# Performance work log

Measured on AMD Instinct MI355X. Metric: run time of the kernel, lower is better.

## Reference

```python
import jax, jax.numpy as jnp
import numpy as np

E = 1_000_000      # number of edges
T = 2_000_000      # number of angle triplets
EDGE_DIM = 64
HIDDEN = 128
LN_EPS = 1e-5


def _layer_norm(x, gamma, beta):
    mu = jnp.mean(x, axis=-1, keepdims=True)
    var = jnp.mean(jnp.square(x - mu), axis=-1, keepdims=True)
    return (x - mu) * jax.lax.rsqrt(var + LN_EPS) * gamma + beta


def setup_inputs() -> dict:
    key = jax.random.key(0)
    ks = jax.random.split(key, 8)
    in_dim = 2 * EDGE_DIM + 4  # 132

    def lin(k, fan_in, fan_out):
        bound = 1.0 / np.sqrt(fan_in)
        kw, kb = jax.random.split(k)
        W = jax.random.uniform(kw, (fan_in, fan_out), jnp.float32, -bound, bound)
        b = jax.random.uniform(kb, (fan_out,), jnp.float32, -bound, bound)
        return W, b

    W1, b1 = lin(ks[0], in_dim, HIDDEN)
    W2, b2 = lin(ks[1], HIDDEN, HIDDEN)
    W3, b3 = lin(ks[2], HIDDEN, EDGE_DIM)

    return {
        "edge_feat": jax.random.normal(ks[3], (E, EDGE_DIM), jnp.float32),
        "triplet_idx": jax.random.randint(ks[4], (T, 2), 0, E, jnp.int64) if jax.config.jax_enable_x64 else jax.random.randint(ks[4], (T, 2), 0, E, jnp.int32),
        "triplet_geo": jax.random.uniform(ks[5], (T, 4), jnp.float32),
        "W1": W1, "b1": b1,
        "g1": jnp.ones((HIDDEN,), jnp.float32), "be1": jnp.zeros((HIDDEN,), jnp.float32),
        "W2": W2, "b2": b2,
        "g2": jnp.ones((HIDDEN,), jnp.float32), "be2": jnp.zeros((HIDDEN,), jnp.float32),
        "W3": W3, "b3": b3,
        "gn": jnp.ones((EDGE_DIM,), jnp.float32), "bn": jnp.zeros((EDGE_DIM,), jnp.float32),
    }


def reference(edge_feat, triplet_idx, triplet_geo,
              W1, b1, g1, be1, W2, b2, g2, be2, W3, b3, gn, bn):
    num_edges = edge_feat.shape[0]
    e_ij = triplet_idx[:, 0]
    e_kj = triplet_idx[:, 1]

    f_ij = edge_feat[e_ij]                      # [T, edge_dim] gather
    f_kj = edge_feat[e_kj]                      # [T, edge_dim] gather
    x = jnp.concatenate([f_ij, f_kj, triplet_geo], axis=1)  # [T, 2*edge_dim+4]

    # mlp_phi: Linear -> SiLU -> LayerNorm -> Linear -> SiLU -> LayerNorm
    h = _layer_norm(jax.nn.silu(x @ W1 + b1), g1, be1)
    m = _layer_norm(jax.nn.silu(h @ W2 + b2), g2, be2)  # [T, hidden]

    # scatter-mean over e_ij with dim_size = num_edges
    sums = jax.ops.segment_sum(m, e_ij, num_segments=num_edges)
    cnts = jax.ops.segment_sum(jnp.ones((m.shape[0],), m.dtype), e_ij, num_segments=num_edges)
    agg = sums / jnp.maximum(cnts, 1.0)[:, None]         # [E, hidden]

    out = edge_feat + (agg @ W3 + b3)
    return _layer_norm(out, gn, bn)
```

## Files before the change

### kernel.cpp

```cpp
#include <hip/hip_runtime.h>
#include <hip/hip_bf16.h>
#include <stdint.h>

typedef __attribute__((ext_vector_type(8))) short short8;
typedef __attribute__((ext_vector_type(4))) float f32x4;
typedef unsigned short u16;

#define OFF_PSUM 0ULL
#define OFF_CNT  256000000ULL
#define OFF_EBF  260000000ULL
#define OFF_WP1  388000000ULL
#define OFF_WP2  (OFF_WP1 + 40960ULL)
#define OFF_WP3  (OFF_WP2 + 32768ULL)
#define OFF_S2   (OFF_WP3 + 16384ULL)
#define OFF_C2   (OFF_S2 + 512ULL)
#define OFF_S3   (OFF_C2 + 512ULL)
#define OFF_T3   (OFF_S3 + 256ULL)

#define LDS_P1S 40960
#define LDS_P1Q 43008
#define LDS_P2S 45056
#define LDS_P2Q 47104
#define LDS_EIJ 49152
#define LDS_EKJ 49664
#define LDS_TOTAL 50176

__device__ __forceinline__ u16 f2bf(float f) {
  union { float f; uint32_t u; } c; c.f = f;
  uint32_t u = c.u;
  return (u16)((u + 0x7FFFu + ((u >> 16) & 1u)) >> 16);
}
__device__ __forceinline__ float silu(float y) {
  return y / (1.0f + __expf(-y));
}

#define MFMA16(a, b, c) __builtin_amdgcn_mfma_f32_16x16x32_bf16((a), (b), (c), 0, 0, 0)


__global__ __launch_bounds__(256) void k_conv_edge(const float* __restrict__ ef,
                                                   u16* __restrict__ ebf) {
  int i = blockIdx.x * 256 + threadIdx.x;
  float4 v = ((const float4*)ef)[i];
  ushort4 o;
  o.x = f2bf(v.x); o.y = f2bf(v.y); o.z = f2bf(v.z); o.w = f2bf(v.w);
  ((ushort4*)ebf)[i] = o;
}

__global__ __launch_bounds__(256) void k_pack_w(const float* __restrict__ W1,
                                                const float* __restrict__ W2,
                                                const float* __restrict__ W3,
                                                const float* __restrict__ g1,
                                                const float* __restrict__ g2,
                                                u16* __restrict__ wp1,
                                                u16* __restrict__ wp2,
                                                u16* __restrict__ wp3) {
  int i = blockIdx.x * 256 + threadIdx.x;
  if (i < 20480) {
    int j = i & 7, n = (i >> 3) & 127, kb = i >> 10;
    int k = kb * 8 + j;
    wp1[i] = (k < 132) ? f2bf(W1[k * 128 + n]) : (u16)0;
  } else if (i < 36864) {
    int i2 = i - 20480;
    int j = i2 & 7, n = (i2 >> 3) & 127, kb = i2 >> 10;
    int k = kb * 8 + j;
    wp2[i2] = f2bf(g1[k] * W2[k * 128 + n]);
  } else if (i < 45056) {
    int i3 = i - 36864;
    int j = i3 & 7, n = (i3 >> 3) & 63, kb = i3 >> 9;
    int k = kb * 8 + j;
    wp3[i3] = f2bf(g2[k] * W3[k * 64 + n]);
  }
}

__global__ __launch_bounds__(256) void k_pack_vec(
    const float* __restrict__ W2, const float* __restrict__ W3,
    const float* __restrict__ g1, const float* __restrict__ be1, const float* __restrict__ b2,
    const float* __restrict__ g2, const float* __restrict__ be2,
    float* __restrict__ s2, float* __restrict__ c2,
    float* __restrict__ s3, float* __restrict__ t3) {
  int t = threadIdx.x;
  if (t < 128) {
    float a = 0.f, b = 0.f;
    for (int k = 0; k < 128; ++k) {
      float w = W2[k * 128 + t];
      a += g1[k] * w; b += be1[k] * w;
    }
    s2[t] = a; c2[t] = b + b2[t];
  } else if (t < 192) {
    int n = t - 128;
    float a = 0.f, b = 0.f;
    for (int k = 0; k < 128; ++k) {
      float w = W3[k * 64 + n];
      a += g2[k] * w; b += be2[k] * w;
    }
    s3[n] = a; t3[n] = b;
  }
}


__global__ __launch_bounds__(512, 4) void k_triplet(
    const u16* __restrict__ ebf, const int* __restrict__ tidx,
    const float* __restrict__ geo,
    const u16* __restrict__ wp1, const u16* __restrict__ wp2, const u16* __restrict__ wp3,
    const float* __restrict__ b1,
    const float* __restrict__ s2v, const float* __restrict__ c2v,
    const float* __restrict__ s3v,
    float* __restrict__ psum, float* __restrict__ cnt) {
  extern __shared__ char smem[];
  float* P1S = (float*)(smem + LDS_P1S);
  float* P1Q = (float*)(smem + LDS_P1Q);
  float* P2S = (float*)(smem + LDS_P2S);
  float* P2Q = (float*)(smem + LDS_P2Q);
  int* EIJ = (int*)(smem + LDS_EIJ);
  int* EKJ = (int*)(smem + LDS_EKJ);

  const int tid = threadIdx.x;
  const int wave = tid >> 6, lane = tid & 63;
  const int wm = wave >> 2, wn = wave & 3;
  const int l15 = lane & 15, lg = lane >> 4;
  const int t0 = blockIdx.x * 128;
  const int n0 = wn * 32 + l15;
  const int n3 = wn * 16 + l15;
  const int rowA = wm * 64 + l15;

  const short8* wb1 = (const short8*)wp1;
  short8 w1f[10];
#pragma unroll
  for (int s5 = 0; s5 < 5; ++s5) {
    int kb = s5 * 4 + lg;
    w1f[2 * s5] = wb1[kb * 128 + n0];
    w1f[2 * s5 + 1] = wb1[kb * 128 + n0 + 16];
  }
  float b1c0 = b1[n0], b1c1 = b1[n0 + 16];

  if (tid < 128) {
    int2 p = ((const int2*)tidx)[t0 + tid];
    EIJ[tid] = p.x; EKJ[tid] = p.y;
    atomicAdd(&cnt[p.x], 1.0f);
  }
  __syncthreads();

  {
    const int r = tid >> 2, s = tid & 3;
    const int e = (s < 2) ? EIJ[r] : EKJ[r];
    const uint4* src = (const uint4*)(ebf + (size_t)e * 64) + (s & 1) * 4;
    uint4 v0 = src[0], v1 = src[1], v2 = src[2], v3 = src[3];
    const int swz = (r & 7) << 4;
    char* rowp = smem + r * 320;
    *(uint4*)(rowp + ((s * 64 + 0) ^ swz)) = v0;
    *(uint4*)(rowp + ((s * 64 + 16) ^ swz)) = v1;
    *(uint4*)(rowp + ((s * 64 + 32) ^ swz)) = v2;
    *(uint4*)(rowp + ((s * 64 + 48) ^ swz)) = v3;
    if (s == 0) {
      float4 gq = ((const float4*)geo)[t0 + r];
      ushort4 gb;
      gb.x = f2bf(gq.x); gb.y = f2bf(gq.y); gb.z = f2bf(gq.z); gb.w = f2bf(gq.w);
      *(ushort4*)(rowp + 256) = gb;
      *(uint2*)(rowp + 264) = (uint2){0, 0};
    } else {
      *(uint4*)(rowp + 256 + s * 16) = (uint4){0, 0, 0, 0};
    }
  }
  __syncthreads();

  f32x4 acc[4][2];
#pragma unroll
  for (int mf = 0; mf < 4; ++mf) { acc[mf][0] = (f32x4)0.f; acc[mf][1] = (f32x4)0.f; }
#pragma unroll
  for (int s5 = 0; s5 < 5; ++s5) {
    short8 a[4];
#pragma unroll
    for (int mf = 0; mf < 4; ++mf) {
      int row = rowA + mf * 16;
      int off = s5 * 64 + lg * 16;
      if (s5 < 4) off ^= (row & 7) << 4;
      a[mf] = *(const short8*)(smem + row * 320 + off);
    }
#pragma unroll
    for (int mf = 0; mf < 4; ++mf) {
      acc[mf][0] = MFMA16(a[mf], w1f[2 * s5], acc[mf][0]);
      acc[mf][1] = MFMA16(a[mf], w1f[2 * s5 + 1], acc[mf][1]);
    }
  }

#pragma unroll
  for (int mf = 0; mf < 4; ++mf)
#pragma unroll
    for (int q = 0; q < 4; ++q) {
      float v0 = silu(acc[mf][0][q] + b1c0);
      float v1 = silu(acc[mf][1][q] + b1c1);
      acc[mf][0][q] = v0; acc[mf][1][q] = v1;
      float ps = v0 + v1, pq = v0 * v0 + v1 * v1;
      ps += __shfl_xor(ps, 1); pq += __shfl_xor(pq, 1);
      ps += __shfl_xor(ps, 2); pq += __shfl_xor(pq, 2);
      ps += __shfl_xor(ps, 4); pq += __shfl_xor(pq, 4);
      ps += __shfl_xor(ps, 8); pq += __shfl_xor(pq, 8);
      if (l15 == 0) {
        int row = wm * 64 + mf * 16 + lg * 4 + q;
        P1S[row * 4 + wn] = ps; P1Q[row * 4 + wn] = pq;
      }
    }
  __syncthreads();

  const short8* wb2 = (const short8*)wp2;
  short8 w2f[8];
#pragma unroll
  for (int s4 = 0; s4 < 4; ++s4) {
    int kb = s4 * 4 + lg;
    w2f[2 * s4] = wb2[kb * 128 + n0];
    w2f[2 * s4 + 1] = wb2[kb * 128 + n0 + 16];
  }
  float s2c0 = s2v[n0], s2c1 = s2v[n0 + 16];
  float c2c0 = c2v[n0], c2c1 = c2v[n0 + 16];

#pragma unroll
  for (int mf = 0; mf < 4; ++mf)
#pragma unroll
    for (int f = 0; f < 2; ++f)
#pragma unroll
      for (int q = 0; q < 4; ++q) {
        int row = wm * 64 + mf * 16 + lg * 4 + q;
        int cb = (wn * 32 + f * 16 + l15) << 1;
        *(u16*)(smem + row * 256 + (cb ^ ((row & 7) << 4))) = f2bf(acc[mf][f][q]);
      }
  __syncthreads();

#pragma unroll
  for (int mf = 0; mf < 4; ++mf) { acc[mf][0] = (f32x4)0.f; acc[mf][1] = (f32x4)0.f; }
#pragma unroll
  for (int s4 = 0; s4 < 4; ++s4) {
    short8 a[4];
#pragma unroll
    for (int mf = 0; mf < 4; ++mf) {
      int row = rowA + mf * 16;
      a[mf] = *(const short8*)(smem + row * 256 + ((s4 * 64 + lg * 16) ^ ((row & 7) << 4)));
    }
#pragma unroll
    for (int mf = 0; mf < 4; ++mf) {
      acc[mf][0] = MFMA16(a[mf], w2f[2 * s4], acc[mf][0]);
      acc[mf][1] = MFMA16(a[mf], w2f[2 * s4 + 1], acc[mf][1]);
    }
  }

#pragma unroll
  for (int mf = 0; mf < 4; ++mf)
#pragma unroll
    for (int q = 0; q < 4; ++q) {
      int row = wm * 64 + mf * 16 + lg * 4 + q;
      float4 sv = *(const float4*)&P1S[row * 4];
      float4 qv = *(const float4*)&P1Q[row * 4];
      float sum = sv.x + sv.y + sv.z + sv.w;
      float sq = qv.x + qv.y + qv.z + qv.w;
      float mu = sum * 0.0078125f;
      float inv = rsqrtf(fmaxf(sq * 0.0078125f - mu * mu, 0.f) + 1e-5f);
      float f0 = inv * (acc[mf][0][q] - mu * s2c0) + c2c0;
      float f1 = inv * (acc[mf][1][q] - mu * s2c1) + c2c1;
      float v0 = silu(f0), v1 = silu(f1);
      acc[mf][0][q] = v0; acc[mf][1][q] = v1;
      float ps = v0 + v1, pq = v0 * v0 + v1 * v1;
      ps += __shfl_xor(ps, 1); pq += __shfl_xor(pq, 1);
      ps += __shfl_xor(ps, 2); pq += __shfl_xor(pq, 2);
      ps += __shfl_xor(ps, 4); pq += __shfl_xor(pq, 4);
      ps += __shfl_xor(ps, 8); pq += __shfl_xor(pq, 8);
      if (l15 == 0) { P2S[row * 4 + wn] = ps; P2Q[row * 4 + wn] = pq; }
    }

  const short8* wb3 = (const short8*)wp3;
  short8 w3f[4];
#pragma unroll
  for (int s4 = 0; s4 < 4; ++s4) w3f[s4] = wb3[(s4 * 4 + lg) * 64 + n3];
  float s3c = s3v[n3];

  __syncthreads();

#pragma unroll
  for (int mf = 0; mf < 4; ++mf)
#pragma unroll
    for (int f = 0; f < 2; ++f)
#pragma unroll
      for (int q = 0; q < 4; ++q) {
        int row = wm * 64 + mf * 16 + lg * 4 + q;
        int cb = (wn * 32 + f * 16 + l15) << 1;
        *(u16*)(smem + row * 256 + (cb ^ ((row & 7) << 4))) = f2bf(acc[mf][f][q]);
      }
  __syncthreads();

  f32x4 acc3[4];
#pragma unroll
  for (int mf = 0; mf < 4; ++mf) acc3[mf] = (f32x4)0.f;
#pragma unroll
  for (int s4 = 0; s4 < 4; ++s4) {
    short8 a[4];
#pragma unroll
    for (int mf = 0; mf < 4; ++mf) {
      int row = rowA + mf * 16;
      a[mf] = *(const short8*)(smem + row * 256 + ((s4 * 64 + lg * 16) ^ ((row & 7) << 4)));
    }
#pragma unroll
    for (int mf = 0; mf < 4; ++mf) acc3[mf] = MFMA16(a[mf], w3f[s4], acc3[mf]);
  }
#pragma unroll
  for (int mf = 0; mf < 4; ++mf)
#pragma unroll
    for (int q = 0; q < 4; ++q) {
      int row = wm * 64 + mf * 16 + lg * 4 + q;
      float4 sv = *(const float4*)&P2S[row * 4];
      float4 qv = *(const float4*)&P2Q[row * 4];
      float sum = sv.x + sv.y + sv.z + sv.w;
      float sq = qv.x + qv.y + qv.z + qv.w;
      float mu = sum * 0.0078125f;
      float inv = rsqrtf(fmaxf(sq * 0.0078125f - mu * mu, 0.f) + 1e-5f);
      float y = inv * (acc3[mf][q] - mu * s3c);
      int e = EIJ[row];
      atomicAdd(psum + (size_t)e * 64 + n3, y);
    }
}


__global__ __launch_bounds__(256) void k_final(
    const float* __restrict__ psum, const float* __restrict__ cnt,
    const float* __restrict__ ef, const float* __restrict__ b3,
    const float* __restrict__ t3, const float* __restrict__ gn,
    const float* __restrict__ bn, float* __restrict__ out) {
  int g = blockIdx.x * 256 + threadIdx.x;
  int e = g >> 2, s = g & 3;
  float cv = cnt[e];
  float ic = 1.0f / fmaxf(cv, 1.0f);
  float tw = (cv > 0.f) ? 1.0f : 0.0f;
  float x[16];
  const float4* ps = (const float4*)(psum + (size_t)e * 64 + s * 16);
  const float4* fe = (const float4*)(ef + (size_t)e * 64 + s * 16);
  const float4* p3 = (const float4*)(b3 + s * 16);
  const float4* pt = (const float4*)(t3 + s * 16);
#pragma unroll
  for (int i = 0; i < 4; ++i) {
    float4 a = ps[i], b = fe[i], c = p3[i], d = pt[i];
    x[4 * i + 0] = b.x + a.x * ic + c.x + tw * d.x;
    x[4 * i + 1] = b.y + a.y * ic + c.y + tw * d.y;
    x[4 * i + 2] = b.z + a.z * ic + c.z + tw * d.z;
    x[4 * i + 3] = b.w + a.w * ic + c.w + tw * d.w;
  }
  float sum = 0.f, ss = 0.f;
#pragma unroll
  for (int i = 0; i < 16; ++i) { sum += x[i]; ss += x[i] * x[i]; }
  sum += __shfl_xor(sum, 1); ss += __shfl_xor(ss, 1);
  sum += __shfl_xor(sum, 2); ss += __shfl_xor(ss, 2);
  float mu = sum * (1.0f / 64.0f);
  float inv = rsqrtf(ss * (1.0f / 64.0f) - mu * mu + 1e-5f);
  float4* po = (float4*)(out + (size_t)e * 64 + s * 16);
#pragma unroll
  for (int i = 0; i < 4; ++i) {
    float4 gv = ((const float4*)(gn + s * 16))[i];
    float4 bv = ((const float4*)(bn + s * 16))[i];
    float4 o;
    o.x = (x[4 * i + 0] - mu) * inv * gv.x + bv.x;
    o.y = (x[4 * i + 1] - mu) * inv * gv.y + bv.y;
    o.z = (x[4 * i + 2] - mu) * inv * gv.z + bv.z;
    o.w = (x[4 * i + 3] - mu) * inv * gv.w + bv.w;
    po[i] = o;
  }
}

extern "C" void kernel_launch(void* const* d_in, const int* in_sizes, int n_in,
                              void* d_out, int out_size, void* d_ws, size_t ws_size,
                              hipStream_t stream) {
  const float* edge_feat = (const float*)d_in[0];
  const int* tidx = (const int*)d_in[1];
  const float* geo = (const float*)d_in[2];
  const float* W1 = (const float*)d_in[3];
  const float* b1 = (const float*)d_in[4];
  const float* g1 = (const float*)d_in[5];
  const float* be1 = (const float*)d_in[6];
  const float* W2 = (const float*)d_in[7];
  const float* b2 = (const float*)d_in[8];
  const float* g2 = (const float*)d_in[9];
  const float* be2 = (const float*)d_in[10];
  const float* W3 = (const float*)d_in[11];
  const float* b3 = (const float*)d_in[12];
  const float* gn = (const float*)d_in[13];
  const float* bn = (const float*)d_in[14];

  char* ws = (char*)d_ws;
  float* psum = (float*)(ws + OFF_PSUM);
  float* cnt = (float*)(ws + OFF_CNT);
  u16* ebf = (u16*)(ws + OFF_EBF);
  u16* wp1 = (u16*)(ws + OFF_WP1);
  u16* wp2 = (u16*)(ws + OFF_WP2);
  u16* wp3 = (u16*)(ws + OFF_WP3);
  float* s2 = (float*)(ws + OFF_S2);
  float* c2 = (float*)(ws + OFF_C2);
  float* s3 = (float*)(ws + OFF_S3);
  float* t3 = (float*)(ws + OFF_T3);
  float* out = (float*)d_out;

  hipMemsetAsync(ws, 0, 260000000ULL, stream);
  k_conv_edge<<<62500, 256, 0, stream>>>(edge_feat, ebf);
  k_pack_w<<<176, 256, 0, stream>>>(W1, W2, W3, g1, g2, wp1, wp2, wp3);
  k_pack_vec<<<1, 256, 0, stream>>>(W2, W3, g1, be1, b2, g2, be2, s2, c2, s3, t3);

  k_triplet<<<15625, 512, LDS_TOTAL, stream>>>(ebf, tidx, geo, wp1, wp2, wp3,
                                               b1, s2, c2, s3, psum, cnt);
  k_final<<<15625, 256, 0, stream>>>(psum, cnt, edge_feat, b3, t3, gn, bn, out);
}
```

Before: 1.077 ms.

## Transpose triplet MLP GEMMs so weights are the A operand and triplets are columns

Restructures the fused triplet MLP so each MFMA treats the weight matrix as the A operand and the triplets as the N dimension. Hidden activations are written to LDS as packed bf16 pairs, and the intermediate layer gets its own buffer, which removes one barrier. LayerNorm statistics now reduce with two cross-lane shuffles instead of four per row. Weights are loaded from global memory inside each k-step instead of being held in registers, and LDS use grows from about 50KB to about 79KB per block, which may lower occupancy. It also switches SiLU to a reciprocal approximation and uses packed bf16 conversion.

```diff
diff --git a/kernel.cpp b/kernel.cpp
--- a/kernel.cpp
+++ b/kernel.cpp
@@ -9,29 +9,37 @@
 #define OFF_PSUM 0ULL
 #define OFF_CNT  256000000ULL
 #define OFF_EBF  260000000ULL
-#define OFF_WP1  388000000ULL
-#define OFF_WP2  (OFF_WP1 + 40960ULL)
-#define OFF_WP3  (OFF_WP2 + 32768ULL)
-#define OFF_S2   (OFF_WP3 + 16384ULL)
+#define OFF_WT1  388000000ULL
+#define OFF_WT2  (OFF_WT1 + 40960ULL)
+#define OFF_WT3  (OFF_WT2 + 32768ULL)
+#define OFF_S2   (OFF_WT3 + 16384ULL)
 #define OFF_C2   (OFF_S2 + 512ULL)
 #define OFF_S3   (OFF_C2 + 512ULL)
 #define OFF_T3   (OFF_S3 + 256ULL)
 
-#define LDS_P1S 40960
-#define LDS_P1Q 43008
-#define LDS_P2S 45056
-#define LDS_P2Q 47104
-#define LDS_EIJ 49152
-#define LDS_EKJ 49664
-#define LDS_TOTAL 50176
+#define LDS_X   0
+#define LDS_H   40960
+#define LDS_P1S 73728
+#define LDS_P1Q 74752
+#define LDS_P2S 75776
+#define LDS_P2Q 76800
+#define LDS_EIJ 77824
+#define LDS_EKJ 78336
+#define LDS_TOTAL 78848
 
 __device__ __forceinline__ u16 f2bf(float f) {
   union { float f; uint32_t u; } c; c.f = f;
   uint32_t u = c.u;
   return (u16)((u + 0x7FFFu + ((u >> 16) & 1u)) >> 16);
 }
+__device__ __forceinline__ uint32_t pkbf(float lo, float hi) {
+  float2 t; t.x = lo; t.y = hi;
+  __hip_bfloat162 h = __float22bfloat162_rn(t);
+  uint32_t u; __builtin_memcpy(&u, &h, 4);
+  return u;
+}
 __device__ __forceinline__ float silu(float y) {
-  return y / (1.0f + __expf(-y));
+  return y * __builtin_amdgcn_rcpf(1.0f + __expf(-y));
 }
 
 #define MFMA16(a, b, c) __builtin_amdgcn_mfma_f32_16x16x32_bf16((a), (b), (c), 0, 0, 0)
@@ -51,24 +59,21 @@
                                                 const float* __restrict__ W3,
                                                 const float* __restrict__ g1,
                                                 const float* __restrict__ g2,
-                                                u16* __restrict__ wp1,
-                                                u16* __restrict__ wp2,
-                                                u16* __restrict__ wp3) {
+                                                u16* __restrict__ wt1,
+                                                u16* __restrict__ wt2,
+                                                u16* __restrict__ wt3) {
   int i = blockIdx.x * 256 + threadIdx.x;
   if (i < 20480) {
-    int j = i & 7, n = (i >> 3) & 127, kb = i >> 10;
-    int k = kb * 8 + j;
-    wp1[i] = (k < 132) ? f2bf(W1[k * 128 + n]) : (u16)0;
+    int n = i / 160, k = i - n * 160;
+    wt1[i] = (k < 132) ? f2bf(W1[k * 128 + n]) : (u16)0;
   } else if (i < 36864) {
     int i2 = i - 20480;
-    int j = i2 & 7, n = (i2 >> 3) & 127, kb = i2 >> 10;
-    int k = kb * 8 + j;
-    wp2[i2] = f2bf(g1[k] * W2[k * 128 + n]);
+    int n = i2 >> 7, k = i2 & 127;
+    wt2[i2] = f2bf(g1[k] * W2[k * 128 + n]);
   } else if (i < 45056) {
     int i3 = i - 36864;
-    int j = i3 & 7, n = (i3 >> 3) & 63, kb = i3 >> 9;
-    int k = kb * 8 + j;
-    wp3[i3] = f2bf(g2[k] * W3[k * 64 + n]);
+    int n = i3 >> 7, k = i3 & 127;
+    wt3[i3] = f2bf(g2[k] * W3[k * 64 + n]);
   }
 }
 
@@ -101,7 +106,7 @@
 __global__ __launch_bounds__(512, 4) void k_triplet(
     const u16* __restrict__ ebf, const int* __restrict__ tidx,
     const float* __restrict__ geo,
-    const u16* __restrict__ wp1, const u16* __restrict__ wp2, const u16* __restrict__ wp3,
+    const u16* __restrict__ wt1, const u16* __restrict__ wt2, const u16* __restrict__ wt3,
     const float* __restrict__ b1,
     const float* __restrict__ s2v, const float* __restrict__ c2v,
     const float* __restrict__ s3v,
@@ -119,19 +124,6 @@
   const int wm = wave >> 2, wn = wave & 3;
   const int l15 = lane & 15, lg = lane >> 4;
   const int t0 = blockIdx.x * 128;
-  const int n0 = wn * 32 + l15;
-  const int n3 = wn * 16 + l15;
-  const int rowA = wm * 64 + l15;
-
-  const short8* wb1 = (const short8*)wp1;
-  short8 w1f[10];
-#pragma unroll
-  for (int s5 = 0; s5 < 5; ++s5) {
-    int kb = s5 * 4 + lg;
-    w1f[2 * s5] = wb1[kb * 128 + n0];
-    w1f[2 * s5 + 1] = wb1[kb * 128 + n0 + 16];
-  }
-  float b1c0 = b1[n0], b1c1 = b1[n0 + 16];
 
   if (tid < 128) {
     int2 p = ((const int2*)tidx)[t0 + tid];
@@ -151,14 +143,16 @@
     *(uint4*)(rowp + ((s * 64 + 16) ^ swz)) = v1;
     *(uint4*)(rowp + ((s * 64 + 32) ^ swz)) = v2;
     *(uint4*)(rowp + ((s * 64 + 48) ^ swz)) = v3;
+    const int tswz = (r & 3) << 4;
     if (s == 0) {
       float4 gq = ((const float4*)geo)[t0 + r];
-      ushort4 gb;
-      gb.x = f2bf(gq.x); gb.y = f2bf(gq.y); gb.z = f2bf(gq.z); gb.w = f2bf(gq.w);
-      *(ushort4*)(rowp + 256) = gb;
-      *(uint2*)(rowp + 264) = (uint2){0, 0};
+      uint2 gw;
+      gw.x = pkbf(gq.x, gq.y); gw.y = pkbf(gq.z, gq.w);
+      char* tp = rowp + 256 + (0 ^ tswz);
+      *(uint2*)tp = gw;
+      *(uint2*)(tp + 8) = (uint2){0, 0};
     } else {
-      *(uint4*)(rowp + 256 + s * 16) = (uint4){0, 0, 0, 0};
+      *(uint4*)(rowp + 256 + ((s * 16) ^ tswz)) = (uint4){0, 0, 0, 0};
     }
   }
   __syncthreads();
@@ -166,154 +160,197 @@
   f32x4 acc[4][2];
 #pragma unroll
   for (int mf = 0; mf < 4; ++mf) { acc[mf][0] = (f32x4)0.f; acc[mf][1] = (f32x4)0.f; }
+  const short8* w1p = (const short8*)wt1;
 #pragma unroll
   for (int s5 = 0; s5 < 5; ++s5) {
-    short8 a[4];
+    short8 aw[4], bx[2];
+#pragma unroll
+    for (int mf = 0; mf < 4; ++mf)
+      aw[mf] = w1p[(wm * 64 + mf * 16 + l15) * 20 + s5 * 4 + lg];
+#pragma unroll
+    for (int f = 0; f < 2; ++f) {
+      int trip = wn * 32 + f * 16 + l15;
+      int off;
+      if (s5 < 4) off = (s5 * 64 + lg * 16) ^ ((trip & 7) << 4);
+      else off = 256 + ((lg * 16) ^ ((trip & 3) << 4));
+      bx[f] = *(const short8*)(smem + trip * 320 + off);
+    }
 #pragma unroll
     for (int mf = 0; mf < 4; ++mf) {
-      int row = rowA + mf * 16;
-      int off = s5 * 64 + lg * 16;
-      if (s5 < 4) off ^= (row & 7) << 4;
-      a[mf] = *(const short8*)(smem + row * 320 + off);
+      acc[mf][0] = MFMA16(aw[mf], bx[0], acc[mf][0]);
+      acc[mf][1] = MFMA16(aw[mf], bx[1], acc[mf][1]);
+    }
+  }
+
+  {
+    float4 b1f[4];
+#pragma unroll
+    for (int mf = 0; mf < 4; ++mf)
+      b1f[mf] = *(const float4*)(b1 + wm * 64 + mf * 16 + lg * 4);
+    float st[2] = {0.f, 0.f}, sq[2] = {0.f, 0.f};
+#pragma unroll
+    for (int mf = 0; mf < 4; ++mf)
+#pragma unroll
+      for (int f = 0; f < 2; ++f)
+#pragma unroll
+        for (int q = 0; q < 4; ++q) {
+          float v = silu(acc[mf][f][q] + b1f[mf][q]);
+          acc[mf][f][q] = v;
+          st[f] += v; sq[f] += v * v;
+        }
+#pragma unroll
+    for (int f = 0; f < 2; ++f) {
+      st[f] += __shfl_xor(st[f], 16); sq[f] += __shfl_xor(sq[f], 16);
+      st[f] += __shfl_xor(st[f], 32); sq[f] += __shfl_xor(sq[f], 32);
+    }
+    if (lg == 0) {
+#pragma unroll
+      for (int f = 0; f < 2; ++f) {
+        int trip = wn * 32 + f * 16 + l15;
+        P1S[trip * 2 + wm] = st[f];
+        P1Q[trip * 2 + wm] = sq[f];
+      }
+    }
+#pragma unroll
+    for (int mf = 0; mf < 4; ++mf)
+#pragma unroll
+      for (int f = 0; f < 2; ++f) {
+        int trip = wn * 32 + f * 16 + l15;
+        uint2 w;
+        w.x = pkbf(acc[mf][f][0], acc[mf][f][1]);
+        w.y = pkbf(acc[mf][f][2], acc[mf][f][3]);
+        *(uint2*)(smem + LDS_H + trip * 256 +
+                  ((wm * 128 + mf * 32 + lg * 8) ^ ((trip & 7) << 4))) = w;
+      }
+  }
+  __syncthreads();
+
+#pragma unroll
+  for (int mf = 0; mf < 4; ++mf) { acc[mf][0] = (f32x4)0.f; acc[mf][1] = (f32x4)0.f; }
+  const short8* w2p = (const short8*)wt2;
+#pragma unroll
+  for (int s4 = 0; s4 < 4; ++s4) {
+    short8 aw[4], bx[2];
+#pragma unroll
+    for (int mf = 0; mf < 4; ++mf)
+      aw[mf] = w2p[(wm * 64 + mf * 16 + l15) * 16 + s4 * 4 + lg];
+#pragma unroll
+    for (int f = 0; f < 2; ++f) {
+      int trip = wn * 32 + f * 16 + l15;
+      bx[f] = *(const short8*)(smem + LDS_H + trip * 256 +
+                               ((s4 * 64 + lg * 16) ^ ((trip & 7) << 4)));
     }
 #pragma unroll
     for (int mf = 0; mf < 4; ++mf) {
-      acc[mf][0] = MFMA16(a[mf], w1f[2 * s5], acc[mf][0]);
-      acc[mf][1] = MFMA16(a[mf], w1f[2 * s5 + 1], acc[mf][1]);
-    }
-  }
-
-#pragma unroll
-  for (int mf = 0; mf < 4; ++mf)
-#pragma unroll
-    for (int q = 0; q < 4; ++q) {
-      float v0 = silu(acc[mf][0][q] + b1c0);
-      float v1 = silu(acc[mf][1][q] + b1c1);
-      acc[mf][0][q] = v0; acc[mf][1][q] = v1;
-      float ps = v0 + v1, pq = v0 * v0 + v1 * v1;
-      ps += __shfl_xor(ps, 1); pq += __shfl_xor(pq, 1);
-      ps += __shfl_xor(ps, 2); pq += __shfl_xor(pq, 2);
-      ps += __shfl_xor(ps, 4); pq += __shfl_xor(pq, 4);
-      ps += __shfl_xor(ps, 8); pq += __shfl_xor(pq, 8);
-      if (l15 == 0) {
-        int row = wm * 64 + mf * 16 + lg * 4 + q;
-        P1S[row * 4 + wn] = ps; P1Q[row * 4 + wn] = pq;
+      acc[mf][0] = MFMA16(aw[mf], bx[0], acc[mf][0]);
+      acc[mf][1] = MFMA16(aw[mf], bx[1], acc[mf][1]);
+    }
+  }
+
+  {
+    float4 s2f[4], c2f[4];
+#pragma unroll
+    for (int mf = 0; mf < 4; ++mf) {
+      s2f[mf] = *(const float4*)(s2v + wm * 64 + mf * 16 + lg * 4);
+      c2f[mf] = *(const float4*)(c2v + wm * 64 + mf * 16 + lg * 4);
+    }
+    float mu[2], inv[2];
+#pragma unroll
+    for (int f = 0; f < 2; ++f) {
+      int trip = wn * 32 + f * 16 + l15;
+      float sm = P1S[trip * 2] + P1S[trip * 2 + 1];
+      float qq = P1Q[trip * 2] + P1Q[trip * 2 + 1];
+      mu[f] = sm * 0.0078125f;
+      inv[f] = rsqrtf(fmaxf(qq * 0.0078125f - mu[f] * mu[f], 0.f) + 1e-5f);
+    }
+    float st[2] = {0.f, 0.f}, sq[2] = {0.f, 0.f};
+#pragma unroll
+    for (int mf = 0; mf < 4; ++mf)
+#pragma unroll
+      for (int f = 0; f < 2; ++f)
+#pragma unroll
+        for (int q = 0; q < 4; ++q) {
+          float y = inv[f] * (acc[mf][f][q] - mu[f] * s2f[mf][q]) + c2f[mf][q];
+          float v = silu(y);
+          acc[mf][f][q] = v;
+          st[f] += v; sq[f] += v * v;
+        }
+#pragma unroll
+    for (int f = 0; f < 2; ++f) {
+      st[f] += __shfl_xor(st[f], 16); sq[f] += __shfl_xor(sq[f], 16);
+      st[f] += __shfl_xor(st[f], 32); sq[f] += __shfl_xor(sq[f], 32);
+    }
+    if (lg == 0) {
+#pragma unroll
+      for (int f = 0; f < 2; ++f) {
+        int trip = wn * 32 + f * 16 + l15;
+        P2S[trip * 2 + wm] = st[f];
+        P2Q[trip * 2 + wm] = sq[f];
       }
     }
+#pragma unroll
+    for (int mf = 0; mf < 4; ++mf)
+#pragma unroll
+      for (int f = 0; f < 2; ++f) {
+        int trip = wn * 32 + f * 16 + l15;
+        uint2 w;
+        w.x = pkbf(acc[mf][f][0], acc[mf][f][1]);
+        w.y = pkbf(acc[mf][f][2], acc[mf][f][3]);
+        *(uint2*)(smem + trip * 256 +
+                  ((wm * 128 + mf * 32 + lg * 8) ^ ((trip & 7) << 4))) = w;
+      }
+  }
   __syncthreads();
 
-  const short8* wb2 = (const short8*)wp2;
-  short8 w2f[8];
+  f32x4 acc3[2][2];
+#pragma unroll
+  for (int mf = 0; mf < 2; ++mf) { acc3[mf][0] = (f32x4)0.f; acc3[mf][1] = (f32x4)0.f; }
+  const short8* w3p = (const short8*)wt3;
 #pragma unroll
   for (int s4 = 0; s4 < 4; ++s4) {
-    int kb = s4 * 4 + lg;
-    w2f[2 * s4] = wb2[kb * 128 + n0];
-    w2f[2 * s4 + 1] = wb2[kb * 128 + n0 + 16];
-  }
-  float s2c0 = s2v[n0], s2c1 = s2v[n0 + 16];
-  float c2c0 = c2v[n0], c2c1 = c2v[n0 + 16];
-
-#pragma unroll
-  for (int mf = 0; mf < 4; ++mf)
-#pragma unroll
-    for (int f = 0; f < 2; ++f)
-#pragma unroll
-      for (int q = 0; q < 4; ++q) {
-        int row = wm * 64 + mf * 16 + lg * 4 + q;
-        int cb = (wn * 32 + f * 16 + l15) << 1;
-        *(u16*)(smem + row * 256 + (cb ^ ((row & 7) << 4))) = f2bf(acc[mf][f][q]);
-      }
-  __syncthreads();
-
-#pragma unroll
-  for (int mf = 0; mf < 4; ++mf) { acc[mf][0] = (f32x4)0.f; acc[mf][1] = (f32x4)0.f; }
-#pragma unroll
-  for (int s4 = 0; s4 < 4; ++s4) {
-    short8 a[4];
-#pragma unroll
-    for (int mf = 0; mf < 4; ++mf) {
-      int row = rowA + mf * 16;
-      a[mf] = *(const short8*)(smem + row * 256 + ((s4 * 64 + lg * 16) ^ ((row & 7) << 4)));
-    }
-#pragma unroll
-    for (int mf = 0; mf < 4; ++mf) {
-      acc[mf][0] = MFMA16(a[mf], w2f[2 * s4], acc[mf][0]);
-      acc[mf][1] = MFMA16(a[mf], w2f[2 * s4 + 1], acc[mf][1]);
-    }
-  }
-
-#pragma unroll
-  for (int mf = 0; mf < 4; ++mf)
-#pragma unroll
-    for (int q = 0; q < 4; ++q) {
-      int row = wm * 64 + mf * 16 + lg * 4 + q;
-      float4 sv = *(const float4*)&P1S[row * 4];
-      float4 qv = *(const float4*)&P1Q[row * 4];
-      float sum = sv.x + sv.y + sv.z + sv.w;
-      float sq = qv.x + qv.y + qv.z + qv.w;
-      float mu = sum * 0.0078125f;
-      float inv = rsqrtf(fmaxf(sq * 0.0078125f - mu * mu, 0.f) + 1e-5f);
-      float f0 = inv * (acc[mf][0][q] - mu * s2c0) + c2c0;
-      float f1 = inv * (acc[mf][1][q] - mu * s2c1) + c2c1;
-      float v0 = silu(f0), v1 = silu(f1);
-      acc[mf][0][q] = v0; acc[mf][1][q] = v1;
-      float ps = v0 + v1, pq = v0 * v0 + v1 * v1;
-      ps += __shfl_xor(ps, 1); pq += __shfl_xor(pq, 1);
-      ps += __shfl_xor(ps, 2); pq += __shfl_xor(pq, 2);
-      ps += __shfl_xor(ps, 4); pq += __shfl_xor(pq, 4);
-      ps += __shfl_xor(ps, 8); pq += __shfl_xor(pq, 8);
-      if (l15 == 0) { P2S[row * 4 + wn] = ps; P2Q[row * 4 + wn] = pq; }
-    }
-
-  const short8* wb3 = (const short8*)wp3;
-  short8 w3f[4];
-#pragma unroll
-  for (int s4 = 0; s4 < 4; ++s4) w3f[s4] = wb3[(s4 * 4 + lg) * 64 + n3];
-  float s3c = s3v[n3];
-
-  __syncthreads();
-
-#pragma unroll
-  for (int mf = 0; mf < 4; ++mf)
-#pragma unroll
-    for (int f = 0; f < 2; ++f)
-#pragma unroll
-      for (int q = 0; q < 4; ++q) {
-        int row = wm * 64 + mf * 16 + lg * 4 + q;
-        int cb = (wn * 32 + f * 16 + l15) << 1;
-        *(u16*)(smem + row * 256 + (cb ^ ((row & 7) << 4))) = f2bf(acc[mf][f][q]);
-      }
-  __syncthreads();
-
-  f32x4 acc3[4];
-#pragma unroll
-  for (int mf = 0; mf < 4; ++mf) acc3[mf] = (f32x4)0.f;
-#pragma unroll
-  for (int s4 = 0; s4 < 4; ++s4) {
-    short8 a[4];
-#pragma unroll
-    for (int mf = 0; mf < 4; ++mf) {
-      int row = rowA + mf * 16;
-      a[mf] = *(const short8*)(smem + row * 256 + ((s4 * 64 + lg * 16) ^ ((row & 7) << 4)));
-    }
-#pragma unroll
-    for (int mf = 0; mf < 4; ++mf) acc3[mf] = MFMA16(a[mf], w3f[s4], acc3[mf]);
-  }
-#pragma unroll
-  for (int mf = 0; mf < 4; ++mf)
-#pragma unroll
-    for (int q = 0; q < 4; ++q) {
-      int row = wm * 64 + mf * 16 + lg * 4 + q;
-      float4 sv = *(const float4*)&P2S[row * 4];
-      float4 qv = *(const float4*)&P2Q[row * 4];
-      float sum = sv.x + sv.y + sv.z + sv.w;
-      float sq = qv.x + qv.y + qv.z + qv.w;
-      float mu = sum * 0.0078125f;
-      float inv = rsqrtf(fmaxf(sq * 0.0078125f - mu * mu, 0.f) + 1e-5f);
-      float y = inv * (acc3[mf][q] - mu * s3c);
-      int e = EIJ[row];
-      atomicAdd(psum + (size_t)e * 64 + n3, y);
-    }
+    short8 aw[2], bx[2];
+#pragma unroll
+    for (int mf = 0; mf < 2; ++mf)
+      aw[mf] = w3p[(wm * 32 + mf * 16 + l15) * 16 + s4 * 4 + lg];
+#pragma unroll
+    for (int f = 0; f < 2; ++f) {
+      int trip = wn * 32 + f * 16 + l15;
+      bx[f] = *(const short8*)(smem + trip * 256 +
+                               ((s4 * 64 + lg * 16) ^ ((trip & 7) << 4)));
+    }
+#pragma unroll
+    for (int mf = 0; mf < 2; ++mf) {
+      acc3[mf][0] = MFMA16(aw[mf], bx[0], acc3[mf][0]);
+      acc3[mf][1] = MFMA16(aw[mf], bx[1], acc3[mf][1]);
+    }
+  }
+  {
+    float4 s3f[2];
+#pragma unroll
+    for (int mf = 0; mf < 2; ++mf)
+      s3f[mf] = *(const float4*)(s3v + wm * 32 + mf * 16 + lg * 4);
+    float mu3[2], inv3[2];
+    int ei[2];
+#pragma unroll
+    for (int f = 0; f < 2; ++f) {
+      int trip = wn * 32 + f * 16 + l15;
+      float sm = P2S[trip * 2] + P2S[trip * 2 + 1];
+      float qq = P2Q[trip * 2] + P2Q[trip * 2 + 1];
+      mu3[f] = sm * 0.0078125f;
+      inv3[f] = rsqrtf(fmaxf(qq * 0.0078125f - mu3[f] * mu3[f], 0.f) + 1e-5f);
+      ei[f] = EIJ[trip];
+    }
+#pragma unroll
+    for (int mf = 0; mf < 2; ++mf)
+#pragma unroll
+      for (int f = 0; f < 2; ++f)
+#pragma unroll
+        for (int q = 0; q < 4; ++q) {
+          float y = inv3[f] * (acc3[mf][f][q] - mu3[f] * s3f[mf][q]);
+          int n3 = wm * 32 + mf * 16 + lg * 4 + q;
+          atomicAdd(psum + (size_t)ei[f] * 64 + n3, y);
+        }
+  }
 }
 
 
@@ -384,9 +421,9 @@
   float* psum = (float*)(ws + OFF_PSUM);
   float* cnt = (float*)(ws + OFF_CNT);
   u16* ebf = (u16*)(ws + OFF_EBF);
-  u16* wp1 = (u16*)(ws + OFF_WP1);
-  u16* wp2 = (u16*)(ws + OFF_WP2);
-  u16* wp3 = (u16*)(ws + OFF_WP3);
+  u16* wt1 = (u16*)(ws + OFF_WT1);
+  u16* wt2 = (u16*)(ws + OFF_WT2);
+  u16* wt3 = (u16*)(ws + OFF_WT3);
   float* s2 = (float*)(ws + OFF_S2);
   float* c2 = (float*)(ws + OFF_C2);
   float* s3 = (float*)(ws + OFF_S3);
@@ -395,10 +432,12 @@
 
   hipMemsetAsync(ws, 0, 260000000ULL, stream);
   k_conv_edge<<<62500, 256, 0, stream>>>(edge_feat, ebf);
-  k_pack_w<<<176, 256, 0, stream>>>(W1, W2, W3, g1, g2, wp1, wp2, wp3);
+  k_pack_w<<<176, 256, 0, stream>>>(W1, W2, W3, g1, g2, wt1, wt2, wt3);
   k_pack_vec<<<1, 256, 0, stream>>>(W2, W3, g1, be1, b2, g2, be2, s2, c2, s3, t3);
 
-  k_triplet<<<15625, 512, LDS_TOTAL, stream>>>(ebf, tidx, geo, wp1, wp2, wp3,
+  hipFuncSetAttribute((const void*)k_triplet,
+                      hipFuncAttributeMaxDynamicSharedMemorySize, LDS_TOTAL);
+  k_triplet<<<15625, 512, LDS_TOTAL, stream>>>(ebf, tidx, geo, wt1, wt2, wt3,
                                                b1, s2, c2, s3, psum, cnt);
   k_final<<<15625, 256, 0, stream>>>(psum, cnt, edge_feat, b3, t3, gn, bn, out);
 }
```

Result: slower. 2.113 ms (+96.2%).
